# Kernel tuning notes

Hardware: AMD Instinct MI355X
Metric: run time of the kernel (lower is better)

Reference implementation:

```python
import jax, jax.numpy as jnp
import numpy as np

TOTAL_WORDS = 10000
EMBED_LEN = 100
SEQ_LEN = 80
BATCH = 2048
UNITS = 1024


def setup_inputs() -> dict:
    key = jax.random.key(0)
    ks = jax.random.split(key, 8)
    inputs = jax.random.randint(ks[0], (BATCH, SEQ_LEN), 0, TOTAL_WORDS)
    s = 0.02
    emb = jax.random.normal(ks[1], (TOTAL_WORDS, EMBED_LEN), jnp.float32) * s
    W0 = jax.random.normal(ks[2], (EMBED_LEN, 4 * UNITS), jnp.float32) * s
    U0 = jax.random.normal(ks[3], (UNITS, 4 * UNITS), jnp.float32) * s
    b0 = jnp.zeros((4 * UNITS,), jnp.float32)
    W1 = jax.random.normal(ks[4], (UNITS, 4 * UNITS), jnp.float32) * s
    U1 = jax.random.normal(ks[5], (UNITS, 4 * UNITS), jnp.float32) * s
    b1 = jnp.zeros((4 * UNITS,), jnp.float32)
    fcW = jax.random.normal(ks[6], (UNITS, 1), jnp.float32) * s
    fcb = jnp.zeros((1,), jnp.float32)
    return {"inputs": inputs, "emb": emb, "W0": W0, "U0": U0, "b0": b0,
            "W1": W1, "U1": U1, "b1": b1, "fcW": fcW, "fcb": fcb}


def _lstm_step(x, h, c, W, U, b):
    # Keras LSTMCell gate order: i, f, g(candidate), o
    z = x @ W + h @ U + b  # [B, 4*units]
    i, f, g, o = jnp.split(z, 4, axis=-1)
    i = jax.nn.sigmoid(i)
    f = jax.nn.sigmoid(f)
    g = jnp.tanh(g)
    o = jax.nn.sigmoid(o)
    c_new = f * c + i * g
    h_new = o * jnp.tanh(c_new)
    return h_new, c_new


def reference(inputs, emb, W0, U0, b0, W1, U1, b1, fcW, fcb):
    x = emb[inputs]                      # [B, T, E]
    xs = jnp.transpose(x, (1, 0, 2))     # [T, B, E] for scan over time
    B = inputs.shape[0]
    U = U0.shape[0]
    init = (jnp.zeros((B, U), x.dtype), jnp.zeros((B, U), x.dtype),
            jnp.zeros((B, U), x.dtype), jnp.zeros((B, U), x.dtype))

    def step(carry, xt):
        h0, c0, h1, c1 = carry
        h0, c0 = _lstm_step(xt, h0, c0, W0, U0, b0)
        h1, c1 = _lstm_step(h0, h1, c1, W1, U1, b1)
        return (h0, c0, h1, c1), None

    (h0, c0, h1, c1), _ = jax.lax.scan(step, init, xs)
    logits = h1 @ fcW + fcb              # [B, 1]
    return jax.nn.sigmoid(logits)
```

## Files before the change

kernel.cpp:

```cpp
#include <hip/hip_runtime.h>

#define DEVI __device__ __forceinline__

typedef __attribute__((ext_vector_type(4))) float f4;
typedef long long i64t;

DEVI unsigned char f2fp8(float x) {
  int p = __builtin_amdgcn_cvt_pk_fp8_f32(x, x, 0, false);
  return (unsigned char)(p & 0xff);
}
DEVI float fp82f(unsigned char b) {
  return __builtin_amdgcn_cvt_f32_fp8((int)b, 0);
}
DEVI float sigmoidf_(float x) { return 1.f / (1.f + __expf(-x)); }
DEVI float tanhf_(float x) {
  float ax = fabsf(x);
  float e = __expf(-2.f * ax);
  float t = (1.f - e) / (1.f + e);
  return x < 0.f ? -t : t;
}

#define GLDS16(g, l) __builtin_amdgcn_global_load_lds( \
    (const __attribute__((address_space(1))) void*)(g), \
    (__attribute__((address_space(3))) void*)(l), 16, 0, 0)

#define SCALE_UP 64.0f
#define SCALE_DN (1.0f / 4096.0f)


__global__ void k_conv_emb(const float* __restrict__ emb, unsigned char* __restrict__ ep) {
  int i = blockIdx.x * 256 + threadIdx.x;
  if (i >= 10000 * 128) return;
  int r = i >> 7, c = i & 127;
  ep[i] = (c < 100) ? f2fp8(emb[r * 100 + c] * SCALE_UP) : (unsigned char)0;
}

DEVI int permn(int n) {
  int g = n >> 10, u = n & 1023;
  return (u >> 5) * 128 + ((u >> 4) & 1) * 64 + g * 16 + (u & 15);
}
DEVI int kswz(int klog, int row) {
  return (klog & ~63) | (((((klog >> 3) & 7) ^ ((row >> 1) & 7))) << 3) | (klog & 7);
}

__global__ void k_conv_w0(const float* __restrict__ W0, const float* __restrict__ U0,
                          unsigned char* __restrict__ WT) {
  int i = blockIdx.x * 256 + threadIdx.x;
  if (i >= 4096 * 1152) return;
  int n = i / 1152, k = i - n * 1152;
  float v;
  if (k < 100) v = W0[k * 4096 + n];
  else if (k < 128) v = 0.f;
  else v = U0[(k - 128) * 4096 + n];
  int np = permn(n);
  WT[(size_t)np * 1152 + kswz(k, np)] = f2fp8(v * SCALE_UP);
}

__global__ void k_conv_w1(const float* __restrict__ W1, const float* __restrict__ U1,
                          unsigned char* __restrict__ WT) {
  int i = blockIdx.x * 256 + threadIdx.x;
  if (i >= 4096 * 2048) return;
  int n = i >> 11, k = i & 2047;
  float v = (k < 1024) ? W1[k * 4096 + n] : U1[(k - 1024) * 4096 + n];
  int np = permn(n);
  WT[(size_t)np * 2048 + kswz(k, np)] = f2fp8(v * SCALE_UP);
}


template<int K1, int KTOT, bool GATHER>
DEVI void lstm_body(int tile, char* smem,
    const unsigned char* __restrict__ src1,
    const unsigned char* __restrict__ src2,
    const int* __restrict__ idx, int t,
    const unsigned char* __restrict__ WT,
    const float* __restrict__ bias,
    float* __restrict__ cbuf,
    unsigned char* __restrict__ hout)
{
  const int tid = threadIdx.x;
  const int bn = tile & 31;
  const int bm = tile >> 5;
  const int m0 = bm * 256;
  const int n0 = bn * 128;

  const int lr = tid >> 2;
  const int c16 = (tid & 3) * 16;
  const int csw = (((tid & 3) ^ ((tid >> 3) & 3))) * 16;

  const unsigned char* g1[2];
  if (GATHER) {
#pragma unroll
    for (int p = 0; p < 2; ++p) {
      int w = idx[(m0 + p * 128 + lr) * 80 + t];
      g1[p] = src1 + (size_t)w * K1 + csw;
    }
  }

  char* const LA0 = smem;
  char* const LB0 = smem + 16384;
  char* const LA1 = smem + 24576;
  char* const LB1 = smem + 40960;

  auto stage = [&](int kb) {
    char* la = (kb & 1) ? LA1 : LA0;
    char* lb = (kb & 1) ? LB1 : LB0;
    const int kc = kb * 64;
    if (GATHER && kc < K1) {
#pragma unroll
      for (int p = 0; p < 2; ++p)
        GLDS16(g1[p] + kc, la + p * 8192 + tid * 16);
    } else {
#pragma unroll
      for (int p = 0; p < 2; ++p) {
        size_t row = (size_t)(m0 + p * 128 + lr);
        const unsigned char* g = (kc < K1)
            ? (src1 + row * 1024 + kc + c16)
            : (src2 + row * 1024 + (kc - K1) + c16);
        GLDS16(g, la + p * 8192 + tid * 16);
      }
    }
    GLDS16(WT + (size_t)(n0 + lr) * KTOT + kc + c16, lb + tid * 16);
  };

  const int lane = tid & 63;
  const int wv = tid >> 6;
  const int wm = wv >> 1;
  const int wn = wv & 1;
  const int cl = lane & 15;
  const int qd = lane >> 4;
  const int qh = qd >> 1, qb = qd & 1;
  const int g8s = (cl >> 1) & 7;
  const int ko8_0 = ((0 + qd) ^ g8s) << 3;
  const int ko8_1 = ((4 + qd) ^ g8s) << 3;
  const int g4s = (cl >> 1) & 3;
  const int ko16_0 = ((qh ^ g4s) << 4) + qb * 8;
  const int ko16_1 = (((2 + qh) ^ g4s) << 4) + qb * 8;

  f4 acc[4][4];
  const f4 fz = {0.f, 0.f, 0.f, 0.f};
#pragma unroll
  for (int a = 0; a < 4; ++a)
#pragma unroll
    for (int b = 0; b < 4; ++b) acc[a][b] = fz;

  stage(0);

  constexpr int NKB = KTOT / 64;
#pragma unroll 1
  for (int kb = 0; kb < NKB; ++kb) {
    __syncthreads();
    if (kb + 1 < NKB) stage(kb + 1);
    char* la = (kb & 1) ? LA1 : LA0;
    char* lb = (kb & 1) ? LB1 : LB0;
    const bool A16 = GATHER && (kb * 64) < K1;
    const int koA0 = A16 ? ko16_0 : ko8_0;
    const int koA1 = A16 ? ko16_1 : ko8_1;
#pragma unroll
    for (int kk = 0; kk < 2; ++kk) {
      const int koA = kk ? koA1 : koA0;
      const int koB = kk ? ko8_1 : ko8_0;
      i64t af[4], bfr[4];
#pragma unroll
      for (int mi = 0; mi < 4; ++mi)
        af[mi] = *(const i64t*)(la + (wm * 64 + mi * 16 + cl) * 64 + koA);
#pragma unroll
      for (int j = 0; j < 4; ++j)
        bfr[j] = *(const i64t*)(lb + (wn * 64 + j * 16 + cl) * 64 + koB);
#pragma unroll
      for (int mi = 0; mi < 4; ++mi)
#pragma unroll
        for (int j = 0; j < 4; ++j)
          acc[mi][j] = __builtin_amdgcn_mfma_f32_16x16x32_fp8_fp8(
              af[mi], bfr[j], acc[mi][j], 0, 0, 0);
    }
  }

  const int u = bn * 32 + wn * 16 + cl;
  const int uhi = u & ~63;
  const int uc8 = (u >> 3) & 7;
  const int ulo = u & 7;
  const float bi = bias[u];
  const float bff = bias[1024 + u];
  const float bg = bias[2048 + u];
  const float bo = bias[3072 + u];
#pragma unroll
  for (int mi = 0; mi < 4; ++mi) {
    int mbase = m0 + wm * 64 + mi * 16 + qd * 4;
#pragma unroll
    for (int r = 0; r < 4; ++r) {
      int m = mbase + r;
      int fm = (qd * 2 + (r >> 1)) & 7;
      int hcol = uhi | ((uc8 ^ fm) << 3) | ulo;
      float gi = sigmoidf_(acc[mi][0][r] * SCALE_DN + bi);
      float gf = sigmoidf_(acc[mi][1][r] * SCALE_DN + bff);
      float gg = tanhf_(acc[mi][2][r] * SCALE_DN + bg);
      float go = sigmoidf_(acc[mi][3][r] * SCALE_DN + bo);
      size_t coff = (size_t)m * 1024 + u;
      float cn = gf * cbuf[coff] + gi * gg;
      cbuf[coff] = cn;
      hout[(size_t)m * 1024 + hcol] = f2fp8(go * tanhf_(cn) * SCALE_UP);
    }
  }
}

__global__ __launch_bounds__(512, 4) void k_step(
    int mode,
    const unsigned char* embp, const unsigned char* h0in,
    const int* idx, int t,
    const unsigned char* WT0, const float* b0, float* c0, unsigned char* h0out,
    const unsigned char* h0prev, const unsigned char* h1in,
    const unsigned char* WT1, const float* b1, float* c1, unsigned char* h1out)
{
  extern __shared__ char smem[];
  const int blk = blockIdx.x;
  int tile;
  bool isL0;
  if (mode == 1) {
    int hi = (blk >> 8) & 1;
    isL0 = ((blk & 1) ^ hi) != 0;
    tile = hi * 128 + ((blk & 255) >> 1);
  } else {
    tile = blk;
    isL0 = (mode == 0);
  }
  if (isL0)
    lstm_body<128, 1152, true>(tile, smem, embp, h0in, idx, t,
                               WT0, b0, c0, h0out);
  else
    lstm_body<1024, 2048, false>(tile, smem, h0prev, h1in, nullptr, 0,
                                 WT1, b1, c1, h1out);
}


__global__ void k_fc(const unsigned char* __restrict__ h1,
                     const float* __restrict__ fcW, const float* __restrict__ fcb,
                     float* __restrict__ out) {
  int wv = threadIdx.x >> 6;
  int lane = threadIdx.x & 63;
  int row = blockIdx.x * 4 + wv;
  if (row >= 2048) return;
  const unsigned char* hr = h1 + (size_t)row * 1024;
  const int f = (row >> 1) & 7;
  float s = 0.f;
  for (int k = lane; k < 1024; k += 64) {
    int ks = (k & ~63) | ((((k >> 3) & 7) ^ f) << 3) | (k & 7);
    s += fp82f(hr[ks]) * fcW[k];
  }
#pragma unroll
  for (int off = 32; off > 0; off >>= 1) s += __shfl_down(s, off);
  if (lane == 0) out[row] = sigmoidf_(s * (1.0f / SCALE_UP) + fcb[0]);
}


extern "C" void kernel_launch(void* const* d_in, const int* in_sizes, int n_in,
                              void* d_out, int out_size, void* d_ws, size_t ws_size,
                              hipStream_t stream) {
  const int*   idx = (const int*)d_in[0];
  const float* emb = (const float*)d_in[1];
  const float* W0  = (const float*)d_in[2];
  const float* U0  = (const float*)d_in[3];
  const float* b0  = (const float*)d_in[4];
  const float* W1  = (const float*)d_in[5];
  const float* U1  = (const float*)d_in[6];
  const float* b1  = (const float*)d_in[7];
  const float* fcW = (const float*)d_in[8];
  const float* fcb = (const float*)d_in[9];
  float* out = (float*)d_out;

  char* ws = (char*)d_ws;
  unsigned char* embp = (unsigned char*)(ws);
  unsigned char* WT0  = (unsigned char*)(ws + 1280000);
  unsigned char* WT1  = (unsigned char*)(ws + 5998592);
  unsigned char* h0b[2] = {(unsigned char*)(ws + 14387200),
                           (unsigned char*)(ws + 16484352)};
  unsigned char* h1b[2] = {(unsigned char*)(ws + 18581504),
                           (unsigned char*)(ws + 20678656)};
  float* c0 = (float*)(ws + 22775808);
  float* c1 = (float*)(ws + 31164416);

  hipMemsetAsync(ws + 14387200, 0, 25165824, stream);

  k_conv_emb<<<5000, 256, 0, stream>>>(emb, embp);
  k_conv_w0<<<18432, 256, 0, stream>>>(W0, U0, WT0);
  k_conv_w1<<<32768, 256, 0, stream>>>(W1, U1, WT1);

  k_step<<<256, 512, 49152, stream>>>(0, embp, h0b[1], idx, 0,
                                      WT0, b0, c0, h0b[0],
                                      nullptr, nullptr, WT1, b1, c1, nullptr);
  for (int t = 1; t < 80; ++t) {
    k_step<<<512, 512, 49152, stream>>>(1, embp, h0b[(t + 1) & 1], idx, t,
                                        WT0, b0, c0, h0b[t & 1],
                                        h0b[(t - 1) & 1], h1b[t & 1],
                                        WT1, b1, c1, h1b[(t + 1) & 1]);
  }
  k_step<<<256, 512, 49152, stream>>>(2, nullptr, nullptr, nullptr, 0,
                                      WT0, b0, c0, nullptr,
                                      h0b[1], h1b[0], WT1, b1, c1, h1b[1]);

  k_fc<<<512, 256, 0, stream>>>(h1b[1], fcW, fcb, out);
}
```

Measured before the change: 4.062 ms.

## Unroll K-loop by two with fixed LDS buffers, hoist addresses, remap tile order

The fp8 MFMA K-loop is unrolled by two, so each half uses a fixed LDS double buffer and needs no per-iteration buffer select. The global address bases for the A and W tiles are hoisted out of the staging lambda. The block-to-tile mapping is also permuted: consecutive blocks now step through the bm/bn tile grid in a different order, which changes which blocks run concurrently and may improve L2/cache reuse of weight or activation tiles. The change adds code size and assumes an even number of K blocks.

```diff
diff --git a/kernel.cpp b/kernel.cpp
--- a/kernel.cpp
+++ b/kernel.cpp
@@ -96,14 +96,22 @@
     }
   }
 
+  const unsigned char* wbase = WT + (size_t)(n0 + lr) * KTOT + c16;
+  const unsigned char* a1b[2];
+  const unsigned char* a2b[2];
+#pragma unroll
+  for (int p = 0; p < 2; ++p) {
+    size_t row = (size_t)(m0 + p * 128 + lr);
+    a1b[p] = src1 + row * 1024 + c16;
+    a2b[p] = src2 + row * 1024 + c16 - K1;
+  }
+
   char* const LA0 = smem;
   char* const LB0 = smem + 16384;
   char* const LA1 = smem + 24576;
   char* const LB1 = smem + 40960;
 
-  auto stage = [&](int kb) {
-    char* la = (kb & 1) ? LA1 : LA0;
-    char* lb = (kb & 1) ? LB1 : LB0;
+  auto stage = [&](int kb, char* la, char* lb) {
     const int kc = kb * 64;
     if (GATHER && kc < K1) {
 #pragma unroll
@@ -112,14 +120,12 @@
     } else {
 #pragma unroll
       for (int p = 0; p < 2; ++p) {
-        size_t row = (size_t)(m0 + p * 128 + lr);
-        const unsigned char* g = (kc < K1)
-            ? (src1 + row * 1024 + kc + c16)
-            : (src2 + row * 1024 + (kc - K1) + c16);
+        const unsigned char* g = (!GATHER && kc < K1) ? a1b[p] + kc
+                                                      : a2b[p] + kc;
         GLDS16(g, la + p * 8192 + tid * 16);
       }
     }
-    GLDS16(WT + (size_t)(n0 + lr) * KTOT + kc + c16, lb + tid * 16);
+    GLDS16(wbase + kc, lb + tid * 16);
   };
 
   const int lane = tid & 63;
@@ -143,18 +149,7 @@
 #pragma unroll
     for (int b = 0; b < 4; ++b) acc[a][b] = fz;
 
-  stage(0);
-
-  constexpr int NKB = KTOT / 64;
-#pragma unroll 1
-  for (int kb = 0; kb < NKB; ++kb) {
-    __syncthreads();
-    if (kb + 1 < NKB) stage(kb + 1);
-    char* la = (kb & 1) ? LA1 : LA0;
-    char* lb = (kb & 1) ? LB1 : LB0;
-    const bool A16 = GATHER && (kb * 64) < K1;
-    const int koA0 = A16 ? ko16_0 : ko8_0;
-    const int koA1 = A16 ? ko16_1 : ko8_1;
+  auto compute = [&](char* la, char* lb, int koA0, int koA1) {
 #pragma unroll
     for (int kk = 0; kk < 2; ++kk) {
       const int koA = kk ? koA1 : koA0;
@@ -172,6 +167,27 @@
         for (int j = 0; j < 4; ++j)
           acc[mi][j] = __builtin_amdgcn_mfma_f32_16x16x32_fp8_fp8(
               af[mi], bfr[j], acc[mi][j], 0, 0, 0);
+    }
+  };
+
+  stage(0, LA0, LB0);
+
+  constexpr int NKB = KTOT / 64;
+  static_assert(NKB % 2 == 0, "K-loop unroll-2 requires even NKB");
+#pragma unroll 1
+  for (int kbp = 0; kbp < NKB / 2; ++kbp) {
+    const int kb0 = kbp * 2;
+    __syncthreads();
+    stage(kb0 + 1, LA1, LB1);
+    {
+      const bool A16 = GATHER && (kb0 * 64) < K1;
+      compute(LA0, LB0, A16 ? ko16_0 : ko8_0, A16 ? ko16_1 : ko8_1);
+    }
+    __syncthreads();
+    if (kb0 + 2 < NKB) stage(kb0 + 2, LA0, LB0);
+    {
+      const bool A16 = GATHER && ((kb0 + 1) * 64) < K1;
+      compute(LA1, LB1, A16 ? ko16_0 : ko8_0, A16 ? ko16_1 : ko8_1);
     }
   }
 
@@ -216,11 +232,11 @@
   int tile;
   bool isL0;
   if (mode == 1) {
-    int hi = (blk >> 8) & 1;
-    isL0 = ((blk & 1) ^ hi) != 0;
-    tile = hi * 128 + ((blk & 255) >> 1);
+    int s = blk >> 3;
+    isL0 = ((s & 1) ^ (s >> 5)) != 0;
+    tile = (blk & 7) * 32 + (s & 31);
   } else {
-    tile = blk;
+    tile = (blk & 7) * 32 + (blk >> 3);
     isL0 = (mode == 0);
   }
   if (isL0)
```

Measured after the change: 4.028 ms. Within noise of the previous version (-0.8%).

## Triple-buffer GEMM staging with vmcnt-based waits and precomputed load addresses

Applied to the files above, without the earlier changes.

Replaces the double-buffered LDS pipeline with a three-stage ring that prefetches two k-blocks ahead. It uses s_waitcnt vmcnt(3) plus a raw barrier instead of __syncthreads, so later loads stay in flight while earlier tiles are consumed. Global source addresses are hoisted out of the stage lambda, and the k-loop is fully unrolled. LDS per block grows to 72KB, which can reduce blocks per CU, and correctness depends on the async-load count assumptions in the vmcnt wait.

```diff
diff --git a/kernel.cpp b/kernel.cpp
--- a/kernel.cpp
+++ b/kernel.cpp
@@ -96,14 +96,20 @@
     }
   }
 
-  char* const LA0 = smem;
-  char* const LB0 = smem + 16384;
-  char* const LA1 = smem + 24576;
-  char* const LB1 = smem + 40960;
-
-  auto stage = [&](int kb) {
-    char* la = (kb & 1) ? LA1 : LA0;
-    char* lb = (kb & 1) ? LB1 : LB0;
+  const unsigned char* wbase = WT + (size_t)(n0 + lr) * KTOT + c16;
+  const unsigned char* a1b[2];
+  const unsigned char* a2b[2];
+#pragma unroll
+  for (int p = 0; p < 2; ++p) {
+    size_t row = (size_t)(m0 + p * 128 + lr);
+    a1b[p] = src1 + row * 1024 + c16;
+    a2b[p] = src2 + row * 1024 + c16 - K1;
+  }
+
+  char* const SAs[3] = {smem, smem + 24576, smem + 49152};
+
+  auto stage = [&](int kb, char* la) {
+    char* lb = la + 16384;
     const int kc = kb * 64;
     if (GATHER && kc < K1) {
 #pragma unroll
@@ -112,14 +118,12 @@
     } else {
 #pragma unroll
       for (int p = 0; p < 2; ++p) {
-        size_t row = (size_t)(m0 + p * 128 + lr);
-        const unsigned char* g = (kc < K1)
-            ? (src1 + row * 1024 + kc + c16)
-            : (src2 + row * 1024 + (kc - K1) + c16);
+        const unsigned char* g = (!GATHER && kc < K1) ? a1b[p] + kc
+                                                      : a2b[p] + kc;
         GLDS16(g, la + p * 8192 + tid * 16);
       }
     }
-    GLDS16(WT + (size_t)(n0 + lr) * KTOT + kc + c16, lb + tid * 16);
+    GLDS16(wbase + kc, lb + tid * 16);
   };
 
   const int lane = tid & 63;
@@ -143,18 +147,8 @@
 #pragma unroll
     for (int b = 0; b < 4; ++b) acc[a][b] = fz;
 
-  stage(0);
-
-  constexpr int NKB = KTOT / 64;
-#pragma unroll 1
-  for (int kb = 0; kb < NKB; ++kb) {
-    __syncthreads();
-    if (kb + 1 < NKB) stage(kb + 1);
-    char* la = (kb & 1) ? LA1 : LA0;
-    char* lb = (kb & 1) ? LB1 : LB0;
-    const bool A16 = GATHER && (kb * 64) < K1;
-    const int koA0 = A16 ? ko16_0 : ko8_0;
-    const int koA1 = A16 ? ko16_1 : ko8_1;
+  auto compute = [&](char* la, int koA0, int koA1) {
+    char* lb = la + 16384;
 #pragma unroll
     for (int kk = 0; kk < 2; ++kk) {
       const int koA = kk ? koA1 : koA0;
@@ -173,6 +167,22 @@
           acc[mi][j] = __builtin_amdgcn_mfma_f32_16x16x32_fp8_fp8(
               af[mi], bfr[j], acc[mi][j], 0, 0, 0);
     }
+  };
+
+  stage(0, SAs[0]);
+  stage(1, SAs[1]);
+
+  constexpr int NKB = KTOT / 64;
+#pragma unroll
+  for (int kb = 0; kb < NKB; ++kb) {
+    if (kb < NKB - 1)
+      asm volatile("s_waitcnt vmcnt(3)" ::: "memory");
+    else
+      asm volatile("s_waitcnt vmcnt(0)" ::: "memory");
+    __builtin_amdgcn_s_barrier();
+    if (kb + 2 < NKB) stage(kb + 2, SAs[(kb + 2) % 3]);
+    const bool A16 = GATHER && (kb * 64) < K1;
+    compute(SAs[kb % 3], A16 ? ko16_0 : ko8_0, A16 ? ko16_1 : ko8_1);
   }
 
   const int u = bn * 32 + wn * 16 + cl;
@@ -284,16 +294,16 @@
   k_conv_w0<<<18432, 256, 0, stream>>>(W0, U0, WT0);
   k_conv_w1<<<32768, 256, 0, stream>>>(W1, U1, WT1);
 
-  k_step<<<256, 512, 49152, stream>>>(0, embp, h0b[1], idx, 0,
+  k_step<<<256, 512, 73728, stream>>>(0, embp, h0b[1], idx, 0,
                                       WT0, b0, c0, h0b[0],
                                       nullptr, nullptr, WT1, b1, c1, nullptr);
   for (int t = 1; t < 80; ++t) {
-    k_step<<<512, 512, 49152, stream>>>(1, embp, h0b[(t + 1) & 1], idx, t,
+    k_step<<<512, 512, 73728, stream>>>(1, embp, h0b[(t + 1) & 1], idx, t,
                                         WT0, b0, c0, h0b[t & 1],
                                         h0b[(t - 1) & 1], h1b[t & 1],
                                         WT1, b1, c1, h1b[(t + 1) & 1]);
   }
-  k_step<<<256, 512, 49152, stream>>>(2, nullptr, nullptr, nullptr, 0,
+  k_step<<<256, 512, 73728, stream>>>(2, nullptr, nullptr, nullptr, 0,
                                       WT0, b0, c0, nullptr,
                                       h0b[1], h1b[0], WT1, b1, c1, h1b[1]);
 
```

After: 3.647 ms, median of 2. -10.2%, faster.
